# Performance work log

Measured on AMD Instinct MI355X. Metric: run time of the kernel, lower is better.

Reference implementation:

```python
import jax, jax.numpy as jnp
import numpy as np

B, T, S, H, E, V, M = 64, 59, 32, 512, 300, 34004, 1024  # batch, dec steps, enc len, hidden, embed, vocab, enc dim (bi)


def setup_inputs() -> dict:
    key = jax.random.key(0)
    ks = jax.random.split(key, 14)
    w = lambda k, sh, sc=0.05: jax.random.normal(k, sh, jnp.float32) * sc
    return dict(
        dec_input=jax.random.randint(ks[0], (B, T), 0, V),
        enc_output=w(ks[1], (B, S, M), 1.0),
        enc_h=w(ks[2], (B, H), 1.0),
        enc_c=w(ks[3], (B, H), 1.0),
        embedding=w(ks[4], (V, E)),
        Wx=w(ks[5], (E + H, 4 * H)),   # LSTM input kernel (input = [emb; prev_attention])
        Uh=w(ks[6], (H, 4 * H)),       # LSTM recurrent kernel
        b=jnp.zeros((4 * H,), jnp.float32),
        Wm=w(ks[7], (M, H)),           # Bahdanau memory layer
        Wq=w(ks[8], (H, H)),           # Bahdanau query layer
        v=w(ks[9], (H,)),              # Bahdanau attention vector
        Wa=w(ks[10], (H + M, H)),      # attention_layer (Dense, no bias)
        Wf=w(ks[11], (H, V)),          # output projection to vocab
        bf=jnp.zeros((V,), jnp.float32),
    )


def reference(dec_input, enc_output, enc_h, enc_c, embedding, Wx, Uh, b, Wm, Wq, v, Wa, Wf, bf):
    # Precompute attention keys once: [B,S,H]
    keys = jnp.einsum('bsm,mh->bsh', enc_output, Wm)
    emb = embedding[dec_input]            # [B,T,E] teacher-forced inputs
    emb_t = jnp.swapaxes(emb, 0, 1)       # [T,B,E]

    def step(carry, x_t):
        h, c, attn = carry
        x = jnp.concatenate([x_t, attn], axis=-1)          # [B,E+H]
        z = x @ Wx + h @ Uh + b                            # [B,4H]
        i, f, g, o = jnp.split(z, 4, axis=-1)              # keras gate order i,f,c,o
        c2 = jax.nn.sigmoid(f) * c + jax.nn.sigmoid(i) * jnp.tanh(g)
        h2 = jax.nn.sigmoid(o) * jnp.tanh(c2)
        # Bahdanau attention: score = v . tanh(keys + Wq q)
        q = h2 @ Wq                                        # [B,H]
        scores = jnp.einsum('h,bsh->bs', v, jnp.tanh(keys + q[:, None, :]))
        align = jax.nn.softmax(scores, axis=-1)            # full memory (seq_len == S)
        ctx = jnp.einsum('bs,bsm->bm', align, enc_output)  # [B,M]
        attn2 = jnp.concatenate([h2, ctx], axis=-1) @ Wa   # attention_layer, [B,H]
        logits = attn2 @ Wf + bf                           # [B,V]
        return (h2, c2, attn2), logits

    init = (enc_h, enc_c, jnp.zeros((B, H), enc_h.dtype))
    _, logits = jax.lax.scan(step, init, emb_t)            # [T,B,V]
    return jnp.swapaxes(logits, 0, 1)                      # [B,T,V]
```

## Files before the change

kernel.cpp:

```cpp
#include <hip/hip_runtime.h>
#include <hip/hip_bf16.h>
#include <cstdint>
#include <cstddef>

typedef unsigned short u16;
typedef unsigned long long u64;
typedef short s8v __attribute__((ext_vector_type(8)));
typedef float f4v __attribute__((ext_vector_type(4)));

#define DI __device__ __forceinline__

DI u16 f2bf(float f){ unsigned u = __float_as_uint(f); u += 0x7fffu + ((u>>16)&1u); return (u16)(u>>16); }
DI float bf2f(u16 h){ return __uint_as_float(((unsigned)h)<<16); }
DI int ocol(int pc){ return ((pc>>3)&3)*512 + (pc>>5)*8 + (pc&7); }
DI int ocol2(int s){ int pc = (s & ~31) | ((s&3)<<3) | ((s>>2)&7); return ocol(pc); }
DI int pc2slot(int pc){ return (pc & ~31) | ((pc&7)<<2) | ((pc>>3)&3); }
DI float sigm(float x){ x = fminf(fmaxf(x,-30.f),30.f); return 1.f/(1.f+__expf(-x)); }
DI float tanhx(float x){ x = fminf(fmaxf(x,-15.f),15.f); float e = __expf(-2.f*x); return (1.f-e)/(1.f+e); }
DI uint4 packh8(const u16* h){
  uint4 r; r.x=(unsigned)h[0]|((unsigned)h[1]<<16); r.y=(unsigned)h[2]|((unsigned)h[3]<<16);
  r.z=(unsigned)h[4]|((unsigned)h[5]<<16); r.w=(unsigned)h[6]|((unsigned)h[7]<<16); return r;
}
DI void unp8(uint4 w, float* o){
  o[0]=bf2f((u16)(w.x&0xffffu)); o[1]=bf2f((u16)(w.x>>16));
  o[2]=bf2f((u16)(w.y&0xffffu)); o[3]=bf2f((u16)(w.y>>16));
  o[4]=bf2f((u16)(w.z&0xffffu)); o[5]=bf2f((u16)(w.z>>16));
  o[6]=bf2f((u16)(w.w&0xffffu)); o[7]=bf2f((u16)(w.w>>16));
}
DI s8v u4s8(uint4 u){ union{uint4 a; s8v b;} t; t.a=u; return t.b; }

DI unsigned cohld32(const void* p){
  return __hip_atomic_load((const unsigned*)p, __ATOMIC_RELAXED, __HIP_MEMORY_SCOPE_AGENT);
}
DI u64 cohld64(const void* p){
  return __hip_atomic_load((const u64*)p, __ATOMIC_RELAXED, __HIP_MEMORY_SCOPE_AGENT);
}
DI f4v cohldf4(const float* p){
  u64 lo = cohld64(p);
  u64 hi = cohld64(p + 2);
  f4v r;
  r[0]=__uint_as_float((unsigned)lo); r[1]=__uint_as_float((unsigned)(lo>>32));
  r[2]=__uint_as_float((unsigned)hi); r[3]=__uint_as_float((unsigned)(hi>>32));
  return r;
}
DI void cohst32(void* p, unsigned v){
  __hip_atomic_store((unsigned*)p, v, __ATOMIC_RELAXED, __HIP_MEMORY_SCOPE_AGENT);
}
DI void cohst64(void* p, u64 v){
  __hip_atomic_store((u64*)p, v, __ATOMIC_RELAXED, __HIP_MEMORY_SCOPE_AGENT);
}

__global__ void k_init(const float* bb, const float* eh, const float* ec,
                       float* bp, float* h2X, float* cst, float* ctxX, unsigned* flags){
  int i = blockIdx.x*256 + threadIdx.x;
  if (i < 2048) bp[i] = bb[ocol2(i)];
  else if (i < 2048+32768) h2X[i-2048] = eh[i-2048];
  else if (i < 2048+65536) cst[i-34816] = ec[i-34816];
  else if (i < 2048+131072) ctxX[i-67584] = 0.f;
  else if (i < 2048+131072+30208) flags[i-133120] = 0u;
}

__global__ void k_hinit(const float* __restrict__ eh, u16* __restrict__ hhi, u16* __restrict__ hlo){
  int i = blockIdx.x*256 + threadIdx.x; if (i >= 64*1536) return;
  int c = i % 1536;
  float f = (c < 512) ? eh[(i/1536)*512 + c] : 0.f;
  u16 hi = f2bf(f);
  hhi[i] = hi;
  hlo[i] = (c < 512) ? f2bf(f - bf2f(hi)) : (u16)0;
}

__global__ void k_cvt(const float* __restrict__ src, u16* __restrict__ dst, int octs){
  int g = blockIdx.x*256 + threadIdx.x; if (g >= octs) return;
  const float4* p = (const float4*)(src + (size_t)g*8);
  float4 a = p[0], b = p[1];
  u16 h[8] = {f2bf(a.x),f2bf(a.y),f2bf(a.z),f2bf(a.w),f2bf(b.x),f2bf(b.y),f2bf(b.z),f2bf(b.w)};
  *(uint4*)&dst[(size_t)g*8] = packh8(h);
}

__global__ void k_embgather(const int* __restrict__ dec, const float* __restrict__ emb, u16* __restrict__ dst){
  int g = blockIdx.x*256 + threadIdx.x; if (g >= 3776*40) return;
  int row = g/40, o = g%40;
  int b = row & 63, t = row >> 6;
  int tok = dec[b*59 + t];
  u16 h[8];
  #pragma unroll
  for(int j=0;j<8;++j){ int k = o*8+j; float f = (k<300)? emb[(size_t)tok*300 + k] : 0.f; h[j]=f2bf(f); }
  *(uint4*)&dst[(size_t)row*320 + o*8] = packh8(h);
}

__global__ void k_wmT(const float* __restrict__ Wm, u16* __restrict__ dst){
  int g = blockIdx.x*256 + threadIdx.x; if (g >= 512*128) return;
  int hcol = g/128, o = g%128;
  u16 h[8];
  #pragma unroll
  for(int j=0;j<8;++j){ int m = o*8+j; h[j]=f2bf(Wm[(size_t)m*512 + hcol]); }
  *(uint4*)&dst[(size_t)hcol*1024 + o*8] = packh8(h);
}

__global__ void k_waT(const float* __restrict__ Wa, u16* __restrict__ dst){
  int g = blockIdx.x*256 + threadIdx.x; if (g >= 512*192) return;
  int c = g/192, o = g%192;
  u16 h[8];
  #pragma unroll
  for(int j=0;j<8;++j){ int k = o*8+j; h[j]=f2bf(Wa[(size_t)k*512 + c]); }
  *(uint4*)&dst[(size_t)c*1536 + o*8] = packh8(h);
}

__global__ void k_wxtpT(const float* __restrict__ Wx, u16* __restrict__ dst){
  int g = blockIdx.x*256 + threadIdx.x; if (g >= 2048*40) return;
  int pc = g/40, o = g%40; int oc = ocol2(pc);
  u16 h[8];
  #pragma unroll
  for(int j=0;j<8;++j){ int e = o*8+j; float f = (e<300)? Wx[(size_t)e*2048 + oc] : 0.f; h[j]=f2bf(f); }
  *(uint4*)&dst[(size_t)pc*320 + o*8] = packh8(h);
}

__global__ void k_wxaT(const float* __restrict__ Wx, u16* __restrict__ dst){
  int g = blockIdx.x*256 + threadIdx.x; if (g >= 2048*192) return;
  int pc = g/192, o = g%192; int oc = ocol(pc);
  u16 h[8];
  #pragma unroll
  for(int j=0;j<8;++j){
    int kp = o*8+j; int seg = kp>>9; int jd = kp&511;
    float f = Wx[(size_t)(300+jd)*2048 + oc];
    u16 hi = f2bf(f);
    h[j] = (seg==2) ? f2bf(f - bf2f(hi)) : hi;
  }
  *(uint4*)&dst[(size_t)pc*1536 + o*8] = packh8(h);
}

__global__ void k_waA(const float* __restrict__ Wa, u16* __restrict__ dst){
  int g = blockIdx.x*256 + threadIdx.x; if (g >= 1536*192) return;
  int r = g/192, o = g%192;
  u16 h[8];
  #pragma unroll
  for(int j=0;j<8;++j){
    int kp = o*8+j; int seg = kp>>9; int jd = kp&511;
    float f = Wa[(size_t)r*512 + jd];
    u16 hi = f2bf(f);
    h[j] = (seg==1) ? f2bf(f - bf2f(hi)) : hi;
  }
  *(uint4*)&dst[(size_t)r*1536 + o*8] = packh8(h);
}

__global__ void k_buhT(const float* __restrict__ Uh, u16* __restrict__ dst){
  int g = blockIdx.x*256 + threadIdx.x; if (g >= 2048*128) return;
  int pc = g/128, o = g%128; int oc = ocol(pc);
  u16 h[8];
  #pragma unroll
  for(int j=0;j<8;++j){
    int kp = o*8+j; int r = kp&511;
    float f = Uh[(size_t)r*2048 + oc];
    u16 hi = f2bf(f);
    h[j] = (kp<512) ? hi : f2bf(f - bf2f(hi));
  }
  *(uint4*)&dst[(size_t)pc*1024 + o*8] = packh8(h);
}

__global__ void k_wzcT(const float* __restrict__ wzcT, const float* __restrict__ Uh, u16* __restrict__ dst){
  int g = blockIdx.x*256 + threadIdx.x; if (g >= 2048*384) return;
  int pc = g/384, o = g%384; int oc = ocol(pc);
  u16 h[8];
  #pragma unroll
  for(int j=0;j<8;++j){
    int kp = o*8+j; int r = kp % 1536;
    float f = wzcT[(size_t)pc*1536 + r] + ((r<512) ? Uh[(size_t)r*2048 + oc] : 0.f);
    u16 hi = f2bf(f);
    h[j] = (kp<1536) ? hi : f2bf(f - bf2f(hi));
  }
  *(uint4*)&dst[(size_t)pc*3072 + o*8] = packh8(h);
}

__global__ void k_a2dump(const float* __restrict__ h2X, const float* __restrict__ ctxX, u16* __restrict__ dst){
  int g = blockIdx.x*256 + threadIdx.x; if (g >= 3776*192) return;
  int r = g/192, o = g%192;
  u16 h[8];
  #pragma unroll
  for(int j=0;j<8;++j){
    int k = o*8+j;
    float f = (k<512) ? h2X[(size_t)(r+64)*512 + k] : ctxX[(size_t)(r+64)*1024 + (k-512)];
    h[j] = f2bf(f);
  }
  *(uint4*)&dst[(size_t)r*1536 + o*8] = packh8(h);
}

__global__ __launch_bounds__(256) void k_wfT(const float* __restrict__ Wf, u16* __restrict__ WfT){
  __shared__ u16 T[64*72];
  int n0 = blockIdx.x*64, k0 = blockIdx.y*64;
  int tid = threadIdx.x;
  int kl = tid>>2, nq = (tid&3)*16;
  u16 h[16];
  if (n0 + 64 <= 34004){
    const float4* p = (const float4*)(Wf + (size_t)(k0+kl)*34004 + n0 + nq);
    #pragma unroll
    for(int q=0;q<4;++q){ float4 f = p[q]; h[q*4+0]=f2bf(f.x); h[q*4+1]=f2bf(f.y); h[q*4+2]=f2bf(f.z); h[q*4+3]=f2bf(f.w); }
  } else {
    #pragma unroll
    for(int j=0;j<16;++j){ int n = n0+nq+j; float f = (n<34004)? Wf[(size_t)(k0+kl)*34004 + n] : 0.f; h[j]=f2bf(f); }
  }
  *(uint4*)&T[kl*72 + nq] = packh8(h);
  *(uint4*)&T[kl*72 + nq + 8] = packh8(h+8);
  __syncthreads();
  int nl = tid>>2, kq = (tid&3)*16;
  int n = n0 + nl;
  if (n < 34004){
    u16 o[16];
    #pragma unroll
    for(int j=0;j<16;++j) o[j] = T[(kq+j)*72 + nl];
    *(uint4*)&WfT[(size_t)n*512 + k0 + kq]     = packh8(o);
    *(uint4*)&WfT[(size_t)n*512 + k0 + kq + 8] = packh8(o+8);
  }
}

template<int EPI>
__global__ __launch_bounds__(256,2) void gemm_bf16(
    const u16* __restrict__ A, const u16* __restrict__ Bt,
    int M, int N, int K,
    float* __restrict__ Cf, u16* __restrict__ Cb,
    const float* __restrict__ bias, float* __restrict__ Cout){
  __shared__ u16 LSbuf[2*128*40];
  u16* Als = LSbuf;
  u16* Bls = LSbuf + 128*40;
  int tid = threadIdx.x;
  int c0 = blockIdx.x*128, r0 = blockIdx.y*128;
  int wid = tid>>6, wr = wid>>1, wc = wid&1;
  int l15 = tid&15, l4 = (tid>>4)&3;
  f4v acc[4][4];
  #pragma unroll
  for(int m=0;m<4;++m)
  #pragma unroll
  for(int n=0;n<4;++n)
  #pragma unroll
  for(int i=0;i<4;++i) acc[m][n][i] = 0.f;

  int r = tid>>1, hf = tid&1;
  size_t arow = (size_t)min(r0 + r, M-1);
  size_t brow = (size_t)min(c0 + r, N-1);
  const u16* abase = A  + arow*K + hf*16;
  const u16* bbase = Bt + brow*K + hf*16;
  int nk = K >> 5;
  uint4 a0 = ((const uint4*)abase)[0], a1 = ((const uint4*)abase)[1];
  uint4 b0 = ((const uint4*)bbase)[0], b1 = ((const uint4*)bbase)[1];
  for (int ch=0; ch<nk; ++ch){
    __syncthreads();
    *(uint4*)&Als[r*40 + hf*16]     = a0;
    *(uint4*)&Als[r*40 + hf*16 + 8] = a1;
    *(uint4*)&Bls[r*40 + hf*16]     = b0;
    *(uint4*)&Bls[r*40 + hf*16 + 8] = b1;
    __syncthreads();
    if (ch+1 < nk){
      const uint4* ap = (const uint4*)(abase + (ch+1)*32);
      const uint4* bp = (const uint4*)(bbase + (ch+1)*32);
      a0 = ap[0]; a1 = ap[1]; b0 = bp[0]; b1 = bp[1];
    }
    s8v af[4], bfr[4];
    #pragma unroll
    for(int m=0;m<4;++m) af[m]  = *(const s8v*)&Als[(wr*64 + m*16 + l15)*40 + l4*8];
    #pragma unroll
    for(int n=0;n<4;++n) bfr[n] = *(const s8v*)&Bls[(wc*64 + n*16 + l15)*40 + l4*8];
    #pragma unroll
    for(int m=0;m<4;++m)
    #pragma unroll
    for(int n=0;n<4;++n)
      acc[m][n] = __builtin_amdgcn_mfma_f32_16x16x32_bf16(af[m], bfr[n], acc[m][n], 0,0,0);
  }
  __syncthreads();
  float* eps = ((float*)LSbuf) + wid*1024;
  #pragma unroll
  for(int m=0;m<4;++m){
    #pragma unroll
    for(int n=0;n<4;++n)
    #pragma unroll
    for(int i=0;i<4;++i)
      eps[(l4*4 + i)*64 + n*16 + l15] = acc[m][n][i];
    #pragma unroll
    for(int q=0;q<4;++q){
      int row = l4 + q*4;
      f4v v = *(const f4v*)&eps[row*64 + l15*4];
      int gr = r0 + wr*64 + m*16 + row;
      int gc = c0 + wc*64 + l15*4;
      if (gr < M && gc < N){
        if constexpr (EPI==0){
          *(f4v*)&Cf[(size_t)gr*N + gc] = v;
        } else if constexpr (EPI==1){
          f4v bv = *(const f4v*)&bias[gc];
          v += bv;
          *(f4v*)&Cf[(size_t)gr*N + gc] = v;
        } else if constexpr (EPI==2){
          unsigned p0 = ((unsigned)f2bf(v[1])<<16) | f2bf(v[0]);
          unsigned p1 = ((unsigned)f2bf(v[3])<<16) | f2bf(v[2]);
          uint2 pk; pk.x = p0; pk.y = p1;
          *(uint2*)&Cb[(size_t)gr*N + gc] = pk;
        } else {
          f4v bv = *(const f4v*)&bias[gc];
          v += bv;
          int b_ = gr&63, tt = gr>>6;
          *(f4v*)&Cout[((size_t)(b_*59 + tt))*34004 + gc] = v;
        }
      }
    }
  }
}

__global__ __launch_bounds__(512,4) void step_fused(
    int t,
    const u16* __restrict__ wzT, const u16* __restrict__ buhT,
    u16* __restrict__ hhi, u16* __restrict__ hlo,
    float* __restrict__ zparts, const float* __restrict__ Zemb,
    float* __restrict__ cst, float* __restrict__ h2X, float* __restrict__ ctxX,
    const u16* __restrict__ wqB, const float* __restrict__ keys,
    const float* __restrict__ enc, const float* __restrict__ vv,
    unsigned* __restrict__ flags){
  __shared__ float smem[16384];
  int bid = blockIdx.x, tid = threadIdx.x;
  unsigned* flg = flags + (size_t)t*512;
  int variant = (t==0) ? 0 : 1;

  if (bid < 256){
    int sl = bid>>6, cg = bid&63;
    int pc0 = cg*32;
    int wv = tid>>6, lane = tid&63;
    int l15 = lane&15, l4 = lane>>4;
    const u16* Bt = variant ? wzT : buhT;
    int physK = variant ? 3072 : 1024;
    int CS = variant ? 36 : 12;
    int ck0 = sl*CS, ck1 = ck0 + CS;

    f4v acc[4][2];
    #pragma unroll
    for(int m=0;m<4;++m)
    #pragma unroll
    for(int n=0;n<2;++n)
    #pragma unroll
    for(int i=0;i<4;++i) acc[m][n][i] = 0.f;

    for (int c = ck0 + wv; c < ck1; c += 8){
      int k1 = c*32;
      const u16* ap; int inner, kB;
      if (variant==0){
        inner = k1 & 511;
        ap = ((((k1>>9)&3)==1) ? hlo : hhi);
        kB = (k1 < 1024) ? (k1 & 511) : (k1 - 512);
      } else {
        int sg = k1/1536; inner = k1 - sg*1536;
        ap = (sg==1) ? hlo : hhi;
        kB = (k1 < 3072) ? (k1 % 1536) : (1536 + (k1 - 3072));
      }
      uint4 av[4], bv[2];
      #pragma unroll
      for(int m=0;m<4;++m)
        av[m] = *(const uint4*)(ap + (size_t)(m*16 + l15)*1536 + inner + l4*8);
      #pragma unroll
      for(int n=0;n<2;++n)
        bv[n] = *(const uint4*)(Bt + (size_t)(pc0 + n*16 + l15)*physK + kB + l4*8);
      #pragma unroll
      for(int m=0;m<4;++m){
        s8v am = u4s8(av[m]);
        #pragma unroll
        for(int n=0;n<2;++n)
          acc[m][n] = __builtin_amdgcn_mfma_f32_16x16x32_bf16(am, u4s8(bv[n]), acc[m][n], 0,0,0);
      }
    }
    float* red = smem + wv*2048;
    #pragma unroll
    for(int m=0;m<4;++m)
    #pragma unroll
    for(int n=0;n<2;++n)
    #pragma unroll
    for(int i=0;i<4;++i)
      red[(m*16 + l4*4 + i)*32 + n*16 + l15] = acc[m][n][i];
    __syncthreads();

    int rr = tid>>3, cq = (tid&7)*4;
    f4v s = *(const f4v*)&smem[rr*32 + cq];
    #pragma unroll
    for(int w=1;w<8;++w)
      s += *(const f4v*)&smem[w*2048 + rr*32 + cq];
    float* zp = zparts + (size_t)sl*131072 + (size_t)rr*2048 + pc0 + cq;
    cohst64(&zp[0], (u64)__float_as_uint(s[0]) | ((u64)__float_as_uint(s[1])<<32));
    cohst64(&zp[2], (u64)__float_as_uint(s[2]) | ((u64)__float_as_uint(s[3])<<32));
    asm volatile("s_waitcnt vmcnt(0)" ::: "memory");
    __syncthreads();
    if (tid==0) cohst32(&flg[bid], 1u);

  } else {
    int b = bid - 256;
    int j = tid;
    int base = (j>>3)*32 + (j&7)*4;
    f4v ze = *(const f4v*)&Zemb[(size_t)t*131072 + (size_t)b*2048 + base];
    float cprev = cst[(size_t)b*512 + j];
    float vvj = vv[j];
    if (b == 0){
      if (tid < 256){
        while (cohld32(&flg[tid]) == 0u) __builtin_amdgcn_s_sleep(2);
      }
      __syncthreads();
      if (tid==0) cohst32(&flg[511], 1u);
    } else {
      if (tid==0){
        while (cohld32(&flg[511]) == 0u) __builtin_amdgcn_s_sleep(1);
      }
      __syncthreads();
    }
    asm volatile("" ::: "memory");

    float* zl  = smem;
    float* h2s = smem + 2048;
    float* vs2 = smem + 2560;
    float* qs  = smem + 3072;
    float* qpl = smem + 3584;
    float* scl = smem + 7680;
    float* alw = smem + 7712;
    {
      int p4 = tid*4;
      f4v z0; z0[0]=0.f; z0[1]=0.f; z0[2]=0.f; z0[3]=0.f;
      #pragma unroll
      for(int s2=0; s2<4; ++s2)
        z0 += cohldf4(&zparts[(size_t)s2*131072 + (size_t)b*2048 + p4]);
      #pragma unroll
      for(int e=0;e<4;++e)
        zl[pc2slot(p4+e)] = z0[e];
    }
    __syncthreads();
    {
      f4v s4 = ze + *(const f4v*)&zl[base];
      float c2 = sigm(s4[1])*cprev + sigm(s4[0])*tanhx(s4[2]);
      float h2 = sigm(s4[3])*tanhx(c2);
      cst[(size_t)b*512 + j] = c2;
      h2X[(size_t)(t+1)*32768 + (size_t)b*512 + j] = h2;
      h2s[j] = h2; vs2[j] = vvj;
      u16 hh2 = f2bf(h2);
      hhi[(size_t)b*1536 + j] = hh2;
      hlo[(size_t)b*1536 + j] = f2bf(h2 - bf2f(hh2));
    }
    __syncthreads();
    {
      int c8 = (tid&63)*8, hs = tid>>6;
      float qp[8] = {0,0,0,0,0,0,0,0};
      for(int hh=0; hh<64; ++hh){
        int h = hs*64 + hh;
        float w[8]; unp8(*(const uint4*)(wqB + (size_t)h*512 + c8), w);
        float hv = h2s[h];
        #pragma unroll
        for(int q=0;q<8;++q) qp[q] += hv*w[q];
      }
      *(float4*)&qpl[hs*512 + c8]     = make_float4(qp[0],qp[1],qp[2],qp[3]);
      *(float4*)&qpl[hs*512 + c8 + 4] = make_float4(qp[4],qp[5],qp[6],qp[7]);
    }
    __syncthreads();
    { float s = 0.f; for(int hs=0; hs<8; ++hs) s += qpl[hs*512 + tid]; qs[tid] = s; }
    __syncthreads();
    {
      int s = tid>>4, hh = tid&15;
      const float4* kb4 = (const float4*)(keys + ((size_t)(b*32 + s))*512 + hh*32);
      float part = 0.f;
      #pragma unroll
      for(int i8=0;i8<8;++i8){
        float4 kv = kb4[i8];
        int h = hh*32 + i8*4;
        part += vs2[h+0]*tanhx(kv.x + qs[h+0]);
        part += vs2[h+1]*tanhx(kv.y + qs[h+1]);
        part += vs2[h+2]*tanhx(kv.z + qs[h+2]);
        part += vs2[h+3]*tanhx(kv.w + qs[h+3]);
      }
      #pragma unroll
      for(int m=1;m<16;m<<=1) part += __shfl_xor(part, m, 64);
      if (hh==0) scl[s] = part;
    }
    __syncthreads();
    if (tid < 32){
      float sc = scl[tid];
      float mx = sc;
      #pragma unroll
      for(int m=1;m<32;m<<=1) mx = fmaxf(mx, __shfl_xor(mx, m, 64));
      float e = __expf(sc - mx);
      float sm = e;
      #pragma unroll
      for(int m=1;m<32;m<<=1) sm += __shfl_xor(sm, m, 64);
      alw[tid] = e/sm;
    }
    __syncthreads();
    {
      const float* eb = enc + (size_t)b*32768;
      int cc = tid*2;
      float c0 = 0.f, c1 = 0.f;
      for(int s=0;s<32;++s){
        float al = alw[s];
        float2 e2 = *(const float2*)&eb[(size_t)s*1024 + cc];
        c0 += al*e2.x;
        c1 += al*e2.y;
      }
      float2 co; co.x = c0; co.y = c1;
      *(float2*)&ctxX[(size_t)(t+1)*65536 + (size_t)b*1024 + cc] = co;
      u16 x0 = f2bf(c0), x1 = f2bf(c1);
      *(unsigned*)&hhi[(size_t)b*1536 + 512 + cc] = (unsigned)x0 | ((unsigned)x1<<16);
      u16 y0 = f2bf(c0 - bf2f(x0)), y1 = f2bf(c1 - bf2f(x1));
      *(unsigned*)&hlo[(size_t)b*1536 + 512 + cc] = (unsigned)y0 | ((unsigned)y1<<16);
    }
  }
}

extern "C" void kernel_launch(void* const* d_in, const int* in_sizes, int n_in,
                              void* d_out, int out_size, void* d_ws, size_t ws_size,
                              hipStream_t stream){
  const int*   dec = (const int*)d_in[0];
  const float* enc = (const float*)d_in[1];
  const float* eh  = (const float*)d_in[2];
  const float* ec  = (const float*)d_in[3];
  const float* emb = (const float*)d_in[4];
  const float* Wx  = (const float*)d_in[5];
  const float* Uh  = (const float*)d_in[6];
  const float* bb  = (const float*)d_in[7];
  const float* Wm  = (const float*)d_in[8];
  const float* Wq  = (const float*)d_in[9];
  const float* vv  = (const float*)d_in[10];
  const float* Wa  = (const float*)d_in[11];
  const float* Wf  = (const float*)d_in[12];
  const float* bf  = (const float*)d_in[13];
  float* out = (float*)d_out;

  char* w = (char*)d_ws; size_t off = 0;
  auto alloc = [&](size_t bytes)->char*{ char* p = w + off; off = (off + bytes + 255) & ~(size_t)255; return p; };
  u16* WfT   = (u16*)alloc((size_t)34004*512*2);
  u16* attn2 = (u16*)alloc((size_t)3776*512*2);
  size_t liveEnd = off;
  const size_t needB = (size_t)131<<20;
  bool fits = (ws_size >= liveEnd + needB);
  char* wb = fits ? (w + liveEnd) : (char*)d_out;
  size_t offb = 0;
  auto allocB = [&](size_t bytes)->char*{ char* p = wb + offb; offb = (offb + bytes + 255) & ~(size_t)255; return p; };

  u16* wzT   = (u16*)allocB((size_t)2048*3072*2);
  u16* buhT  = (u16*)allocB((size_t)2048*1024*2);
  u16* wqB   = (u16*)allocB((size_t)512*512*2);
  u16* waT   = (u16*)allocB((size_t)512*1536*2);
  u16* wmT   = (u16*)allocB((size_t)512*1024*2);
  u16* wxtpT = (u16*)allocB((size_t)2048*320*2);
  u16* wxaT  = (u16*)allocB((size_t)2048*1536*2);
  u16* waA   = (u16*)allocB((size_t)1536*1536*2);
  float* wzc = (float*)allocB((size_t)2048*1536*4);
  u16* embB  = (u16*)allocB((size_t)3776*320*2);
  u16* encB  = (u16*)allocB((size_t)2048*1024*2);
  float* Zemb  = (float*)allocB((size_t)3776*2048*4);
  float* keys  = (float*)allocB((size_t)2048*512*4);
  float* zparts= (float*)allocB((size_t)9*64*2048*4);
  float* h2X   = (float*)allocB((size_t)60*64*512*4);
  float* ctxX  = (float*)allocB((size_t)60*64*1024*4);
  float* cst   = (float*)allocB((size_t)64*512*4);
  float* bp    = (float*)allocB((size_t)2048*4);
  u16* A2c   = (u16*)allocB((size_t)3776*1536*2);
  u16* hhi   = (u16*)allocB((size_t)64*1536*2);
  u16* hlo   = (u16*)allocB((size_t)64*1536*2);
  unsigned* flags = (unsigned*)allocB((size_t)59*512*4);

  k_init<<<638,256,0,stream>>>(bb, eh, ec, bp, h2X, cst, ctxX, flags);
  k_hinit<<<384,256,0,stream>>>(eh, hhi, hlo);
  k_embgather<<<(3776*40+255)/256,256,0,stream>>>(dec, emb, embB);
  k_cvt<<<(262144+255)/256,256,0,stream>>>(enc, encB, 262144);
  k_cvt<<<(32768+255)/256,256,0,stream>>>(Wq, wqB, 32768);
  k_wmT<<<(512*128+255)/256,256,0,stream>>>(Wm, wmT);
  k_waT<<<(512*192+255)/256,256,0,stream>>>(Wa, waT);
  k_wxtpT<<<(2048*40+255)/256,256,0,stream>>>(Wx, wxtpT);
  k_wxaT<<<(2048*192+255)/256,256,0,stream>>>(Wx, wxaT);
  k_buhT<<<(2048*128+255)/256,256,0,stream>>>(Uh, buhT);
  k_waA<<<(1536*192+255)/256,256,0,stream>>>(Wa, waA);
  k_wfT<<<dim3(532,8),256,0,stream>>>(Wf, WfT);

  gemm_bf16<1><<<dim3(16,30),256,0,stream>>>(embB, wxtpT, 3776, 2048, 320, Zemb, nullptr, bp, nullptr);
  gemm_bf16<0><<<dim3(4,16),256,0,stream>>>(encB, wmT, 2048, 512, 1024, keys, nullptr, nullptr, nullptr);
  gemm_bf16<0><<<dim3(12,16),256,0,stream>>>(wxaT, waA, 2048, 1536, 1536, wzc, nullptr, nullptr, nullptr);
  k_wzcT<<<(2048*384+255)/256,256,0,stream>>>(wzc, Uh, wzT);

  for (int t=0; t<59; ++t){
    step_fused<<<320,512,0,stream>>>(t, wzT, buhT, hhi, hlo, zparts, Zemb,
                                     cst, h2X, ctxX, wqB, keys, enc, vv, flags);
  }

  k_a2dump<<<(3776*192+255)/256,256,0,stream>>>(h2X, ctxX, A2c);
  gemm_bf16<2><<<dim3(4,30),256,0,stream>>>(A2c, waT, 3776, 512, 1536, nullptr, attn2, nullptr, nullptr);
  gemm_bf16<3><<<dim3(266,30),256,0,stream>>>(attn2, WfT, 3776, 34004, 512, nullptr, nullptr, bf, out);
}
```

Baseline: 1.918 ms.

## Merge prep kernels, batch setup GEMMs, use fp16 dot2 for query, bf16 context

All weight conversion and transpose kernels are merged into one large launch, and the three setup GEMMs into a single launch, which cuts launch count and lets independent work run together. Inside each step, the Wq query projection now uses fp16 pairs with the fdot2 instruction, and the context reduction reads bf16 encoder outputs instead of fp32. This halves memory traffic and instruction count on the per-step hot path. The cost is lower precision for q (fp16 h and Wq) and for the context (bf16 enc), which may change numerics.

```diff
diff --git a/kernel.cpp b/kernel.cpp
--- a/kernel.cpp
+++ b/kernel.cpp
@@ -1,5 +1,6 @@
 #include <hip/hip_runtime.h>
 #include <hip/hip_bf16.h>
+#include <hip/hip_fp16.h>
 #include <cstdint>
 #include <cstddef>
 
@@ -7,8 +8,15 @@
 typedef unsigned long long u64;
 typedef short s8v __attribute__((ext_vector_type(8)));
 typedef float f4v __attribute__((ext_vector_type(4)));
+typedef _Float16 f16x2 __attribute__((ext_vector_type(2)));
 
 #define DI __device__ __forceinline__
+
+#if defined(__has_builtin)
+#  if __has_builtin(__builtin_amdgcn_fdot2)
+#    define HAS_FDOT2 1
+#  endif
+#endif
 
 DI u16 f2bf(float f){ unsigned u = __float_as_uint(f); u += 0x7fffu + ((u>>16)&1u); return (u16)(u>>16); }
 DI float bf2f(u16 h){ return __uint_as_float(((unsigned)h)<<16); }
@@ -21,13 +29,17 @@
   uint4 r; r.x=(unsigned)h[0]|((unsigned)h[1]<<16); r.y=(unsigned)h[2]|((unsigned)h[3]<<16);
   r.z=(unsigned)h[4]|((unsigned)h[5]<<16); r.w=(unsigned)h[6]|((unsigned)h[7]<<16); return r;
 }
-DI void unp8(uint4 w, float* o){
-  o[0]=bf2f((u16)(w.x&0xffffu)); o[1]=bf2f((u16)(w.x>>16));
-  o[2]=bf2f((u16)(w.y&0xffffu)); o[3]=bf2f((u16)(w.y>>16));
-  o[4]=bf2f((u16)(w.z&0xffffu)); o[5]=bf2f((u16)(w.z>>16));
-  o[6]=bf2f((u16)(w.w&0xffffu)); o[7]=bf2f((u16)(w.w>>16));
-}
 DI s8v u4s8(uint4 u){ union{uint4 a; s8v b;} t; t.a=u; return t.b; }
+
+DI float qdot(unsigned w, f16x2 hv, float acc){
+#ifdef HAS_FDOT2
+  f16x2 wv; __builtin_memcpy(&wv, &w, 4);
+  return __builtin_amdgcn_fdot2(wv, hv, acc, false);
+#else
+  __half2 hp = *reinterpret_cast<const __half2*>(&w);
+  return acc + (float)hv[0]*__half2float(hp.x) + (float)hv[1]*__half2float(hp.y);
+#endif
+}
 
 DI unsigned cohld32(const void* p){
   return __hip_atomic_load((const unsigned*)p, __ATOMIC_RELAXED, __HIP_MEMORY_SCOPE_AGENT);
@@ -50,111 +62,136 @@
   __hip_atomic_store((u64*)p, v, __ATOMIC_RELAXED, __HIP_MEMORY_SCOPE_AGENT);
 }
 
-__global__ void k_init(const float* bb, const float* eh, const float* ec,
-                       float* bp, float* h2X, float* cst, float* ctxX, unsigned* flags){
-  int i = blockIdx.x*256 + threadIdx.x;
-  if (i < 2048) bp[i] = bb[ocol2(i)];
-  else if (i < 2048+32768) h2X[i-2048] = eh[i-2048];
-  else if (i < 2048+65536) cst[i-34816] = ec[i-34816];
-  else if (i < 2048+131072) ctxX[i-67584] = 0.f;
-  else if (i < 2048+131072+30208) flags[i-133120] = 0u;
-}
-
-__global__ void k_hinit(const float* __restrict__ eh, u16* __restrict__ hhi, u16* __restrict__ hlo){
-  int i = blockIdx.x*256 + threadIdx.x; if (i >= 64*1536) return;
-  int c = i % 1536;
-  float f = (c < 512) ? eh[(i/1536)*512 + c] : 0.f;
-  u16 hi = f2bf(f);
-  hhi[i] = hi;
-  hlo[i] = (c < 512) ? f2bf(f - bf2f(hi)) : (u16)0;
-}
-
-__global__ void k_cvt(const float* __restrict__ src, u16* __restrict__ dst, int octs){
-  int g = blockIdx.x*256 + threadIdx.x; if (g >= octs) return;
-  const float4* p = (const float4*)(src + (size_t)g*8);
-  float4 a = p[0], b = p[1];
-  u16 h[8] = {f2bf(a.x),f2bf(a.y),f2bf(a.z),f2bf(a.w),f2bf(b.x),f2bf(b.y),f2bf(b.z),f2bf(b.w)};
-  *(uint4*)&dst[(size_t)g*8] = packh8(h);
-}
-
-__global__ void k_embgather(const int* __restrict__ dec, const float* __restrict__ emb, u16* __restrict__ dst){
-  int g = blockIdx.x*256 + threadIdx.x; if (g >= 3776*40) return;
-  int row = g/40, o = g%40;
-  int b = row & 63, t = row >> 6;
-  int tok = dec[b*59 + t];
-  u16 h[8];
-  #pragma unroll
-  for(int j=0;j<8;++j){ int k = o*8+j; float f = (k<300)? emb[(size_t)tok*300 + k] : 0.f; h[j]=f2bf(f); }
-  *(uint4*)&dst[(size_t)row*320 + o*8] = packh8(h);
-}
-
-__global__ void k_wmT(const float* __restrict__ Wm, u16* __restrict__ dst){
-  int g = blockIdx.x*256 + threadIdx.x; if (g >= 512*128) return;
-  int hcol = g/128, o = g%128;
-  u16 h[8];
-  #pragma unroll
-  for(int j=0;j<8;++j){ int m = o*8+j; h[j]=f2bf(Wm[(size_t)m*512 + hcol]); }
-  *(uint4*)&dst[(size_t)hcol*1024 + o*8] = packh8(h);
-}
-
-__global__ void k_waT(const float* __restrict__ Wa, u16* __restrict__ dst){
-  int g = blockIdx.x*256 + threadIdx.x; if (g >= 512*192) return;
-  int c = g/192, o = g%192;
-  u16 h[8];
-  #pragma unroll
-  for(int j=0;j<8;++j){ int k = o*8+j; h[j]=f2bf(Wa[(size_t)k*512 + c]); }
-  *(uint4*)&dst[(size_t)c*1536 + o*8] = packh8(h);
-}
-
-__global__ void k_wxtpT(const float* __restrict__ Wx, u16* __restrict__ dst){
-  int g = blockIdx.x*256 + threadIdx.x; if (g >= 2048*40) return;
-  int pc = g/40, o = g%40; int oc = ocol2(pc);
-  u16 h[8];
-  #pragma unroll
-  for(int j=0;j<8;++j){ int e = o*8+j; float f = (e<300)? Wx[(size_t)e*2048 + oc] : 0.f; h[j]=f2bf(f); }
-  *(uint4*)&dst[(size_t)pc*320 + o*8] = packh8(h);
-}
-
-__global__ void k_wxaT(const float* __restrict__ Wx, u16* __restrict__ dst){
-  int g = blockIdx.x*256 + threadIdx.x; if (g >= 2048*192) return;
-  int pc = g/192, o = g%192; int oc = ocol(pc);
-  u16 h[8];
-  #pragma unroll
-  for(int j=0;j<8;++j){
-    int kp = o*8+j; int seg = kp>>9; int jd = kp&511;
-    float f = Wx[(size_t)(300+jd)*2048 + oc];
+__global__ __launch_bounds__(256) void k_build(
+    const float* __restrict__ bb, const float* __restrict__ eh, const float* __restrict__ ec,
+    const int* __restrict__ dec, const float* __restrict__ enc, const float* __restrict__ emb,
+    const float* __restrict__ Wx, const float* __restrict__ Uh, const float* __restrict__ Wm,
+    const float* __restrict__ Wq, const float* __restrict__ Wa, const float* __restrict__ Wf,
+    float* __restrict__ bp, float* __restrict__ h2X, float* __restrict__ cst,
+    float* __restrict__ ctxX, unsigned* __restrict__ flags,
+    u16* __restrict__ hhi, u16* __restrict__ hlo, u16* __restrict__ encB,
+    u16* __restrict__ wq2, u16* __restrict__ wmT, u16* __restrict__ waT,
+    u16* __restrict__ wxtpT, u16* __restrict__ wxaT, u16* __restrict__ buhT,
+    u16* __restrict__ waA, u16* __restrict__ embB, u16* __restrict__ WfT){
+  __shared__ u16 T[64*72];
+  int lb = blockIdx.x, tid = threadIdx.x;
+  if (lb < 638){
+    int i = lb*256 + tid;
+    if (i < 2048) bp[i] = bb[ocol2(i)];
+    else if (i < 2048+32768) h2X[i-2048] = eh[i-2048];
+    else if (i < 2048+65536) cst[i-34816] = ec[i-34816];
+    else if (i < 2048+131072) ctxX[i-67584] = 0.f;
+    else if (i < 2048+131072+30208) flags[i-133120] = 0u;
+  } else if (lb < 1022){
+    int i = (lb-638)*256 + tid; if (i >= 64*1536) return;
+    int c = i % 1536;
+    float f = (c < 512) ? eh[(i/1536)*512 + c] : 0.f;
     u16 hi = f2bf(f);
-    h[j] = (seg==2) ? f2bf(f - bf2f(hi)) : hi;
-  }
-  *(uint4*)&dst[(size_t)pc*1536 + o*8] = packh8(h);
-}
-
-__global__ void k_waA(const float* __restrict__ Wa, u16* __restrict__ dst){
-  int g = blockIdx.x*256 + threadIdx.x; if (g >= 1536*192) return;
-  int r = g/192, o = g%192;
-  u16 h[8];
-  #pragma unroll
-  for(int j=0;j<8;++j){
-    int kp = o*8+j; int seg = kp>>9; int jd = kp&511;
-    float f = Wa[(size_t)r*512 + jd];
-    u16 hi = f2bf(f);
-    h[j] = (seg==1) ? f2bf(f - bf2f(hi)) : hi;
-  }
-  *(uint4*)&dst[(size_t)r*1536 + o*8] = packh8(h);
-}
-
-__global__ void k_buhT(const float* __restrict__ Uh, u16* __restrict__ dst){
-  int g = blockIdx.x*256 + threadIdx.x; if (g >= 2048*128) return;
-  int pc = g/128, o = g%128; int oc = ocol(pc);
-  u16 h[8];
-  #pragma unroll
-  for(int j=0;j<8;++j){
-    int kp = o*8+j; int r = kp&511;
-    float f = Uh[(size_t)r*2048 + oc];
-    u16 hi = f2bf(f);
-    h[j] = (kp<512) ? hi : f2bf(f - bf2f(hi));
-  }
-  *(uint4*)&dst[(size_t)pc*1024 + o*8] = packh8(h);
+    hhi[i] = hi;
+    hlo[i] = (c < 512) ? f2bf(f - bf2f(hi)) : (u16)0;
+  } else if (lb < 2046){
+    int g = (lb-1022)*256 + tid; if (g >= 262144) return;
+    const float4* p = (const float4*)(enc + (size_t)g*8);
+    float4 a = p[0], b = p[1];
+    u16 h[8] = {f2bf(a.x),f2bf(a.y),f2bf(a.z),f2bf(a.w),f2bf(b.x),f2bf(b.y),f2bf(b.z),f2bf(b.w)};
+    *(uint4*)&encB[(size_t)g*8] = packh8(h);
+  } else if (lb < 3070){
+    int g = (lb-2046)*256 + tid; if (g >= 262144) return;
+    int h = g>>9, c = g&511;
+    __half hf = __float2half(Wq[g]);
+    wq2[(size_t)(h>>1)*1024 + (c<<1) + (h&1)] = *reinterpret_cast<u16*>(&hf);
+  } else if (lb < 3326){
+    int g = (lb-3070)*256 + tid; if (g >= 512*128) return;
+    int hcol = g/128, o = g%128;
+    u16 h[8];
+    #pragma unroll
+    for(int j=0;j<8;++j){ int m = o*8+j; h[j]=f2bf(Wm[(size_t)m*512 + hcol]); }
+    *(uint4*)&wmT[(size_t)hcol*1024 + o*8] = packh8(h);
+  } else if (lb < 3710){
+    int g = (lb-3326)*256 + tid; if (g >= 512*192) return;
+    int c = g/192, o = g%192;
+    u16 h[8];
+    #pragma unroll
+    for(int j=0;j<8;++j){ int k = o*8+j; h[j]=f2bf(Wa[(size_t)k*512 + c]); }
+    *(uint4*)&waT[(size_t)c*1536 + o*8] = packh8(h);
+  } else if (lb < 4030){
+    int g = (lb-3710)*256 + tid; if (g >= 2048*40) return;
+    int pc = g/40, o = g%40; int oc = ocol2(pc);
+    u16 h[8];
+    #pragma unroll
+    for(int j=0;j<8;++j){ int e = o*8+j; float f = (e<300)? Wx[(size_t)e*2048 + oc] : 0.f; h[j]=f2bf(f); }
+    *(uint4*)&wxtpT[(size_t)pc*320 + o*8] = packh8(h);
+  } else if (lb < 5566){
+    int g = (lb-4030)*256 + tid; if (g >= 2048*192) return;
+    int pc = g/192, o = g%192; int oc = ocol(pc);
+    u16 h[8];
+    #pragma unroll
+    for(int j=0;j<8;++j){
+      int kp = o*8+j; int seg = kp>>9; int jd = kp&511;
+      float f = Wx[(size_t)(300+jd)*2048 + oc];
+      u16 hi = f2bf(f);
+      h[j] = (seg==2) ? f2bf(f - bf2f(hi)) : hi;
+    }
+    *(uint4*)&wxaT[(size_t)pc*1536 + o*8] = packh8(h);
+  } else if (lb < 6590){
+    int g = (lb-5566)*256 + tid; if (g >= 2048*128) return;
+    int pc = g/128, o = g%128; int oc = ocol(pc);
+    u16 h[8];
+    #pragma unroll
+    for(int j=0;j<8;++j){
+      int kp = o*8+j; int r = kp&511;
+      float f = Uh[(size_t)r*2048 + oc];
+      u16 hi = f2bf(f);
+      h[j] = (kp<512) ? hi : f2bf(f - bf2f(hi));
+    }
+    *(uint4*)&buhT[(size_t)pc*1024 + o*8] = packh8(h);
+  } else if (lb < 7742){
+    int g = (lb-6590)*256 + tid; if (g >= 1536*192) return;
+    int r = g/192, o = g%192;
+    u16 h[8];
+    #pragma unroll
+    for(int j=0;j<8;++j){
+      int kp = o*8+j; int seg = kp>>9; int jd = kp&511;
+      float f = Wa[(size_t)r*512 + jd];
+      u16 hi = f2bf(f);
+      h[j] = (seg==1) ? f2bf(f - bf2f(hi)) : hi;
+    }
+    *(uint4*)&waA[(size_t)r*1536 + o*8] = packh8(h);
+  } else if (lb < 8332){
+    int g = (lb-7742)*256 + tid; if (g >= 3776*40) return;
+    int row = g/40, o = g%40;
+    int b = row & 63, t = row >> 6;
+    int tok = dec[b*59 + t];
+    u16 h[8];
+    #pragma unroll
+    for(int j=0;j<8;++j){ int k = o*8+j; float f = (k<300)? emb[(size_t)tok*300 + k] : 0.f; h[j]=f2bf(f); }
+    *(uint4*)&embB[(size_t)row*320 + o*8] = packh8(h);
+  } else {
+    int lb2 = lb - 8332;
+    int n0 = (lb2 % 532)*64, k0 = (lb2/532)*64;
+    int kl = tid>>2, nq = (tid&3)*16;
+    u16 h[16];
+    if (n0 + 64 <= 34004){
+      const float4* p = (const float4*)(Wf + (size_t)(k0+kl)*34004 + n0 + nq);
+      #pragma unroll
+      for(int q=0;q<4;++q){ float4 f = p[q]; h[q*4+0]=f2bf(f.x); h[q*4+1]=f2bf(f.y); h[q*4+2]=f2bf(f.z); h[q*4+3]=f2bf(f.w); }
+    } else {
+      #pragma unroll
+      for(int j=0;j<16;++j){ int n = n0+nq+j; float f = (n<34004)? Wf[(size_t)(k0+kl)*34004 + n] : 0.f; h[j]=f2bf(f); }
+    }
+    *(uint4*)&T[kl*72 + nq] = packh8(h);
+    *(uint4*)&T[kl*72 + nq + 8] = packh8(h+8);
+    __syncthreads();
+    int nl = tid>>2, kq = (tid&3)*16;
+    int n = n0 + nl;
+    if (n < 34004){
+      u16 o[16];
+      #pragma unroll
+      for(int j=0;j<16;++j) o[j] = T[(kq+j)*72 + nl];
+      *(uint4*)&WfT[(size_t)n*512 + k0 + kq]     = packh8(o);
+      *(uint4*)&WfT[(size_t)n*512 + k0 + kq + 8] = packh8(o+8);
+    }
+  }
 }
 
 __global__ void k_wzcT(const float* __restrict__ wzcT, const float* __restrict__ Uh, u16* __restrict__ dst){
@@ -184,45 +221,16 @@
   *(uint4*)&dst[(size_t)r*1536 + o*8] = packh8(h);
 }
 
-__global__ __launch_bounds__(256) void k_wfT(const float* __restrict__ Wf, u16* __restrict__ WfT){
-  __shared__ u16 T[64*72];
-  int n0 = blockIdx.x*64, k0 = blockIdx.y*64;
-  int tid = threadIdx.x;
-  int kl = tid>>2, nq = (tid&3)*16;
-  u16 h[16];
-  if (n0 + 64 <= 34004){
-    const float4* p = (const float4*)(Wf + (size_t)(k0+kl)*34004 + n0 + nq);
-    #pragma unroll
-    for(int q=0;q<4;++q){ float4 f = p[q]; h[q*4+0]=f2bf(f.x); h[q*4+1]=f2bf(f.y); h[q*4+2]=f2bf(f.z); h[q*4+3]=f2bf(f.w); }
-  } else {
-    #pragma unroll
-    for(int j=0;j<16;++j){ int n = n0+nq+j; float f = (n<34004)? Wf[(size_t)(k0+kl)*34004 + n] : 0.f; h[j]=f2bf(f); }
-  }
-  *(uint4*)&T[kl*72 + nq] = packh8(h);
-  *(uint4*)&T[kl*72 + nq + 8] = packh8(h+8);
-  __syncthreads();
-  int nl = tid>>2, kq = (tid&3)*16;
-  int n = n0 + nl;
-  if (n < 34004){
-    u16 o[16];
-    #pragma unroll
-    for(int j=0;j<16;++j) o[j] = T[(kq+j)*72 + nl];
-    *(uint4*)&WfT[(size_t)n*512 + k0 + kq]     = packh8(o);
-    *(uint4*)&WfT[(size_t)n*512 + k0 + kq + 8] = packh8(o+8);
-  }
-}
-
 template<int EPI>
-__global__ __launch_bounds__(256,2) void gemm_bf16(
+DI void gemm_dev(int bx, int by, u16* LSbuf,
     const u16* __restrict__ A, const u16* __restrict__ Bt,
     int M, int N, int K,
     float* __restrict__ Cf, u16* __restrict__ Cb,
     const float* __restrict__ bias, float* __restrict__ Cout){
-  __shared__ u16 LSbuf[2*128*40];
   u16* Als = LSbuf;
   u16* Bls = LSbuf + 128*40;
   int tid = threadIdx.x;
-  int c0 = blockIdx.x*128, r0 = blockIdx.y*128;
+  int c0 = bx*128, r0 = by*128;
   int wid = tid>>6, wr = wid>>1, wc = wid&1;
   int l15 = tid&15, l4 = (tid>>4)&3;
   f4v acc[4][4];
@@ -302,14 +310,42 @@
   }
 }
 
+template<int EPI>
+__global__ __launch_bounds__(256,2) void gemm_bf16(
+    const u16* __restrict__ A, const u16* __restrict__ Bt,
+    int M, int N, int K,
+    float* __restrict__ Cf, u16* __restrict__ Cb,
+    const float* __restrict__ bias, float* __restrict__ Cout){
+  __shared__ u16 LSbuf[2*128*40];
+  gemm_dev<EPI>(blockIdx.x, blockIdx.y, LSbuf, A, Bt, M, N, K, Cf, Cb, bias, Cout);
+}
+
+__global__ __launch_bounds__(256,2) void k_gemm3(
+    const u16* __restrict__ embB, const u16* __restrict__ wxtpT, float* __restrict__ Zemb,
+    const float* __restrict__ bp,
+    const u16* __restrict__ encB, const u16* __restrict__ wmT, float* __restrict__ keys,
+    const u16* __restrict__ wxaT, const u16* __restrict__ waA, float* __restrict__ wzc){
+  __shared__ u16 LSbuf[2*128*40];
+  int b = blockIdx.x;
+  if (b < 480){
+    gemm_dev<1>(b%16, b/16, LSbuf, embB, wxtpT, 3776, 2048, 320, Zemb, nullptr, bp, nullptr);
+  } else if (b < 544){
+    int b2 = b-480;
+    gemm_dev<0>(b2%4, b2/4, LSbuf, encB, wmT, 2048, 512, 1024, keys, nullptr, nullptr, nullptr);
+  } else {
+    int b3 = b-544;
+    gemm_dev<0>(b3%12, b3/12, LSbuf, wxaT, waA, 2048, 1536, 1536, wzc, nullptr, nullptr, nullptr);
+  }
+}
+
 __global__ __launch_bounds__(512,4) void step_fused(
     int t,
     const u16* __restrict__ wzT, const u16* __restrict__ buhT,
     u16* __restrict__ hhi, u16* __restrict__ hlo,
     float* __restrict__ zparts, const float* __restrict__ Zemb,
     float* __restrict__ cst, float* __restrict__ h2X, float* __restrict__ ctxX,
-    const u16* __restrict__ wqB, const float* __restrict__ keys,
-    const float* __restrict__ enc, const float* __restrict__ vv,
+    const u16* __restrict__ wq2, const float* __restrict__ keys,
+    const u16* __restrict__ encB, const float* __restrict__ vv,
     unsigned* __restrict__ flags){
   __shared__ float smem[16384];
   int bid = blockIdx.x, tid = threadIdx.x;
@@ -437,12 +473,18 @@
     {
       int c8 = (tid&63)*8, hs = tid>>6;
       float qp[8] = {0,0,0,0,0,0,0,0};
-      for(int hh=0; hh<64; ++hh){
-        int h = hs*64 + hh;
-        float w[8]; unp8(*(const uint4*)(wqB + (size_t)h*512 + c8), w);
-        float hv = h2s[h];
-        #pragma unroll
-        for(int q=0;q<8;++q) qp[q] += hv*w[q];
+      const u16* wp = wq2 + (size_t)(hs*32)*1024 + c8*2;
+      #pragma unroll 4
+      for(int i=0;i<32;++i){
+        int hp = hs*32 + i;
+        f16x2 hv; hv[0] = (_Float16)h2s[2*hp]; hv[1] = (_Float16)h2s[2*hp+1];
+        uint4 w0 = *(const uint4*)wp;
+        uint4 w1 = *(const uint4*)(wp + 8);
+        wp += 1024;
+        qp[0]=qdot(w0.x,hv,qp[0]); qp[1]=qdot(w0.y,hv,qp[1]);
+        qp[2]=qdot(w0.z,hv,qp[2]); qp[3]=qdot(w0.w,hv,qp[3]);
+        qp[4]=qdot(w1.x,hv,qp[4]); qp[5]=qdot(w1.y,hv,qp[5]);
+        qp[6]=qdot(w1.z,hv,qp[6]); qp[7]=qdot(w1.w,hv,qp[7]);
       }
       *(float4*)&qpl[hs*512 + c8]     = make_float4(qp[0],qp[1],qp[2],qp[3]);
       *(float4*)&qpl[hs*512 + c8 + 4] = make_float4(qp[4],qp[5],qp[6],qp[7]);
@@ -481,14 +523,14 @@
     }
     __syncthreads();
     {
-      const float* eb = enc + (size_t)b*32768;
+      const u16* eb = encB + (size_t)b*32768;
       int cc = tid*2;
       float c0 = 0.f, c1 = 0.f;
       for(int s=0;s<32;++s){
         float al = alw[s];
-        float2 e2 = *(const float2*)&eb[(size_t)s*1024 + cc];
-        c0 += al*e2.x;
-        c1 += al*e2.y;
+        unsigned ev = *(const unsigned*)&eb[(size_t)s*1024 + cc];
+        c0 += al*bf2f((u16)(ev&0xffffu));
+        c1 += al*bf2f((u16)(ev>>16));
       }
       float2 co; co.x = c0; co.y = c1;
       *(float2*)&ctxX[(size_t)(t+1)*65536 + (size_t)b*1024 + cc] = co;
@@ -532,7 +574,7 @@
 
   u16* wzT   = (u16*)allocB((size_t)2048*3072*2);
   u16* buhT  = (u16*)allocB((size_t)2048*1024*2);
-  u16* wqB   = (u16*)allocB((size_t)512*512*2);
+  u16* wq2   = (u16*)allocB((size_t)512*512*2);
   u16* waT   = (u16*)allocB((size_t)512*1536*2);
   u16* wmT   = (u16*)allocB((size_t)512*1024*2);
   u16* wxtpT = (u16*)allocB((size_t)2048*320*2);
@@ -553,27 +595,17 @@
   u16* hlo   = (u16*)allocB((size_t)64*1536*2);
   unsigned* flags = (unsigned*)allocB((size_t)59*512*4);
 
-  k_init<<<638,256,0,stream>>>(bb, eh, ec, bp, h2X, cst, ctxX, flags);
-  k_hinit<<<384,256,0,stream>>>(eh, hhi, hlo);
-  k_embgather<<<(3776*40+255)/256,256,0,stream>>>(dec, emb, embB);
-  k_cvt<<<(262144+255)/256,256,0,stream>>>(enc, encB, 262144);
-  k_cvt<<<(32768+255)/256,256,0,stream>>>(Wq, wqB, 32768);
-  k_wmT<<<(512*128+255)/256,256,0,stream>>>(Wm, wmT);
-  k_waT<<<(512*192+255)/256,256,0,stream>>>(Wa, waT);
-  k_wxtpT<<<(2048*40+255)/256,256,0,stream>>>(Wx, wxtpT);
-  k_wxaT<<<(2048*192+255)/256,256,0,stream>>>(Wx, wxaT);
-  k_buhT<<<(2048*128+255)/256,256,0,stream>>>(Uh, buhT);
-  k_waA<<<(1536*192+255)/256,256,0,stream>>>(Wa, waA);
-  k_wfT<<<dim3(532,8),256,0,stream>>>(Wf, WfT);
-
-  gemm_bf16<1><<<dim3(16,30),256,0,stream>>>(embB, wxtpT, 3776, 2048, 320, Zemb, nullptr, bp, nullptr);
-  gemm_bf16<0><<<dim3(4,16),256,0,stream>>>(encB, wmT, 2048, 512, 1024, keys, nullptr, nullptr, nullptr);
-  gemm_bf16<0><<<dim3(12,16),256,0,stream>>>(wxaT, waA, 2048, 1536, 1536, wzc, nullptr, nullptr, nullptr);
+  k_build<<<12588,256,0,stream>>>(bb, eh, ec, dec, enc, emb, Wx, Uh, Wm, Wq, Wa, Wf,
+                                  bp, h2X, cst, ctxX, flags,
+                                  hhi, hlo, encB, wq2, wmT, waT,
+                                  wxtpT, wxaT, buhT, waA, embB, WfT);
+
+  k_gemm3<<<736,256,0,stream>>>(embB, wxtpT, Zemb, bp, encB, wmT, keys, wxaT, waA, wzc);
   k_wzcT<<<(2048*384+255)/256,256,0,stream>>>(wzc, Uh, wzT);
 
   for (int t=0; t<59; ++t){
     step_fused<<<320,512,0,stream>>>(t, wzT, buhT, hhi, hlo, zparts, Zemb,
-                                     cst, h2X, ctxX, wqB, keys, enc, vv, flags);
+                                     cst, h2X, ctxX, wq2, keys, encB, vv, flags);
   }
 
   k_a2dump<<<(3776*192+255)/256,256,0,stream>>>(h2X, ctxX, A2c);
```

Result: faster. 1.720 ms (-10.3%).
